# Performance work log

Measured on AMD Instinct MI355X. Metric: run time of the kernel, lower is better.

The kernel has to match this reference:

```python
import jax, jax.numpy as jnp
import numpy as np
from jax import lax

B, H, W, C = 8, 128, 128, 256
HEADS, DH, KR = 8, 64, 64
INNER = HEADS * DH  # 512


def setup_inputs() -> dict:
    key = jax.random.key(0)
    ks = jax.random.split(key, 8)
    s = 0.02
    return {
        "x": jax.random.normal(ks[0], (B, H * W, C), jnp.float32),
        "conv_w": jax.random.normal(ks[1], (INNER, C, 3, 3), jnp.float32) * s,
        "conv_b": jnp.zeros((INNER,), jnp.float32),
        "Wq": jax.random.normal(ks[2], (KR, DH), jnp.float32) * s,
        "Wk": jax.random.normal(ks[3], (KR, DH), jnp.float32) * s,
        "Wv": jax.random.normal(ks[4], (DH, DH), jnp.float32) * s,
        "W1": jax.random.normal(ks[5], (C, INNER), jnp.float32) * s,
        "b1": jnp.zeros((C,), jnp.float32),
        "W2": jax.random.normal(ks[6], (C, C), jnp.float32) * s,
        "b2": jnp.zeros((C,), jnp.float32),
    }


def reference(x, conv_w, conv_b, Wq, Wk, Wv, W1, b1, W2, b2):
    Bv, N, Cv = x.shape
    # b (h w) c -> b c h w
    x4 = x.reshape(Bv, H, W, Cv).transpose(0, 3, 1, 2)
    xc = lax.conv_general_dilated(
        x4, conv_w, window_strides=(1, 1), padding="SAME",
        dimension_numbers=("NCHW", "OIHW", "NCHW"))
    xc = xc + conv_b[None, :, None, None]
    # b (nh dh) h w -> b nh (h w) dh
    x_mid = xc.reshape(Bv, HEADS, DH, H * W).transpose(0, 1, 3, 2)
    q = jnp.einsum("bhnd,kd->bhnk", x_mid, Wq)
    k = jnp.einsum("bhnd,kd->bhnk", x_mid, Wk)
    v = jnp.einsum("bhnd,cd->bhnc", x_mid, Wv)
    q = jax.nn.softmax(q, axis=-1)           # over key_ratio dim
    k = jax.nn.softmax(k, axis=-2)           # over sequence dim
    kv = jnp.einsum("bhnd,bhnc->bhdc", k, v)  # [B,H,KR,DH]
    qkv = jnp.einsum("bhnd,bhdc->bhnc", q, kv)
    # b h n d -> b n (h d)
    qkv = qkv.transpose(0, 2, 1, 3).reshape(Bv, N, INNER)
    h = jax.nn.gelu(qkv @ W1.T + b1, approximate=False)
    return h @ W2.T + b2
```

## Files before the change

### kernel.cpp

```cpp
#include <hip/hip_runtime.h>
#include <math.h>

#define BB 8
#define NN 16384
#define CCH 256
#define OCH 512
#define IMG 128

typedef float4 f4;
typedef _Float16 half8 __attribute__((ext_vector_type(8)));
typedef float floatx4 __attribute__((ext_vector_type(4)));

__device__ __forceinline__ f4 ldg4(const float* p) { return *(const f4*)p; }

__device__ __forceinline__ void gl16(const _Float16* g, const _Float16* l) {
  __builtin_amdgcn_global_load_lds(
      (const __attribute__((address_space(1))) void*)g,
      (__attribute__((address_space(3))) void*)l, 16, 0, 0);
}

__global__ __launch_bounds__(256) void pad_split(const float* __restrict__ x,
                                                 _Float16* __restrict__ xh,
                                                 _Float16* __restrict__ xl) {
  int tid = blockIdx.x * 256 + threadIdx.x;
  int c8 = tid & 31;
  int p = tid >> 5;
  int xcol = p % 130;
  int p2 = p / 130;
  int y = p2 % 130;
  int b = p2 / 130;
  half8 hv, lv;
#pragma unroll
  for (int j = 0; j < 8; ++j) { hv[j] = (_Float16)0.f; lv[j] = (_Float16)0.f; }
  if (y >= 1 && y <= 128 && xcol >= 1 && xcol <= 128) {
    const float* src = x + ((size_t)(b * 128 + y - 1) * 128 + (xcol - 1)) * 256 + c8 * 8;
    f4 v0 = ldg4(src);
    f4 v1 = ldg4(src + 4);
    float vv[8] = {v0.x, v0.y, v0.z, v0.w, v1.x, v1.y, v1.z, v1.w};
#pragma unroll
    for (int j = 0; j < 8; ++j) {
      _Float16 h = (_Float16)vv[j];
      hv[j] = h;
      lv[j] = (_Float16)(vv[j] - (float)h);
    }
  }
  size_t dst = (size_t)p * 256 + c8 * 8;
  *(half8*)(xh + dst) = hv;
  *(half8*)(xl + dst) = lv;
}

__global__ __launch_bounds__(256) void wsplit(const float* __restrict__ cw,
                                              _Float16* __restrict__ wh,
                                              _Float16* __restrict__ wl) {
  int tid = blockIdx.x * 256 + threadIdx.x;
  int c8 = tid & 31;
  int o = (tid >> 5) & 511;
  int tap = tid >> 14;
  half8 hv, lv;
#pragma unroll
  for (int j = 0; j < 8; ++j) {
    float v = cw[(size_t)o * 2304 + (c8 * 8 + j) * 9 + tap];
    _Float16 h = (_Float16)v;
    hv[j] = h;
    lv[j] = (_Float16)(v - (float)h);
  }
  size_t dst = ((size_t)tap * 512 + o) * 256 + c8 * 8;
  *(half8*)(wh + dst) = hv;
  *(half8*)(wl + dst) = lv;
}

__global__ __launch_bounds__(256) void conv_mfma(const _Float16* __restrict__ xph,
                                                 const _Float16* __restrict__ xpl,
                                                 const _Float16* __restrict__ wh,
                                                 const _Float16* __restrict__ wl,
                                                 const float* __restrict__ cb,
                                                 float* __restrict__ xc) {
  __shared__ __align__(16) _Float16 sm[32768];
  const int t = threadIdx.x;
  const int w = t >> 6, lane = t & 63;
  const int id = blockIdx.x;
  const int swz = (id & 7) * 512 + (id >> 3);
  const int obase = (swz & 3) * 128;
  const int p = swz >> 2;
  const int bi = p >> 7, yy = p & 127;
  const int wm = (w & 1) * 64, wn = (w >> 1) * 64;

  floatx4 acc[4][4];
#pragma unroll
  for (int i = 0; i < 4; ++i)
#pragma unroll
    for (int j = 0; j < 4; ++j) acc[i][j] = (floatx4){0.f, 0.f, 0.f, 0.f};

  const int g0 = w, g1 = 4 + w;
  const int loff0 = ((g0 & 1) * 64 + lane) * 256 + (g0 >> 1) * 8;
  const int loff1 = ((g1 & 1) * 64 + lane) * 256 + (g1 >> 1) * 8;

  auto stage = [&](int it, int bsel) {
    const int tap = it >> 3;
    const int dy = (tap * 11) >> 5;
    const int dx = tap - dy * 3;
    const int c0 = (it & 7) * 32;
    const size_t ab = (size_t)((bi * 130 + yy + dy) * 130 + dx) * 256 + c0;
    const size_t bb = (size_t)(tap * 512 + obase) * 256 + c0;
    _Float16* smb = sm + bsel * 16384;
    gl16(xph + ab + loff0, smb + g0 * 512);
    gl16(xph + ab + loff1, smb + g1 * 512);
    gl16(xpl + ab + loff0, smb + 4096 + g0 * 512);
    gl16(xpl + ab + loff1, smb + 4096 + g1 * 512);
    gl16(wh + bb + loff0, smb + 8192 + g0 * 512);
    gl16(wh + bb + loff1, smb + 8192 + g1 * 512);
    gl16(wl + bb + loff0, smb + 12288 + g0 * 512);
    gl16(wl + bb + loff1, smb + 12288 + g1 * 512);
  };

  const int kq = (lane >> 4) * 1024;
  const int ar = (wm + (lane & 15)) * 8;
  const int br = (wn + (lane & 15)) * 8;

  stage(0, 0);
  asm volatile("s_waitcnt vmcnt(0)" ::: "memory");
  __builtin_amdgcn_s_barrier();

  int buf = 0;
#pragma unroll 2
  for (int it = 0; it < 72; ++it) {
    if (it < 71) stage(it + 1, buf ^ 1);

    const _Float16* smb = sm + buf * 16384;
    half8 ah[4], al[4], bh[4], bl[4];
#pragma unroll
    for (int mt = 0; mt < 4; ++mt) {
      ah[mt] = *(const half8*)&smb[kq + ar + mt * 128];
      al[mt] = *(const half8*)&smb[4096 + kq + ar + mt * 128];
    }
#pragma unroll
    for (int nt = 0; nt < 4; ++nt) {
      bh[nt] = *(const half8*)&smb[8192 + kq + br + nt * 128];
      bl[nt] = *(const half8*)&smb[12288 + kq + br + nt * 128];
    }

    __builtin_amdgcn_s_setprio(1);
#pragma unroll
    for (int mt = 0; mt < 4; ++mt)
#pragma unroll
      for (int nt = 0; nt < 4; ++nt) {
        acc[mt][nt] = __builtin_amdgcn_mfma_f32_16x16x32_f16(ah[mt], bh[nt], acc[mt][nt], 0, 0, 0);
        acc[mt][nt] = __builtin_amdgcn_mfma_f32_16x16x32_f16(al[mt], bh[nt], acc[mt][nt], 0, 0, 0);
        acc[mt][nt] = __builtin_amdgcn_mfma_f32_16x16x32_f16(ah[mt], bl[nt], acc[mt][nt], 0, 0, 0);
      }
    __builtin_amdgcn_s_setprio(0);
    __builtin_amdgcn_sched_barrier(0);
    asm volatile("s_waitcnt vmcnt(0)" ::: "memory");
    __builtin_amdgcn_s_barrier();
    buf ^= 1;
  }

  const int col = lane & 15;
  const int qr = (lane >> 4) * 4;
#pragma unroll
  for (int nt = 0; nt < 4; ++nt) {
    const int och = obase + wn + nt * 16 + col;
    const float bias = cb[och];
#pragma unroll
    for (int mt = 0; mt < 4; ++mt)
#pragma unroll
      for (int r = 0; r < 4; ++r) {
        int m = wm + mt * 16 + qr + r;
        xc[((size_t)bi * NN + (size_t)yy * IMG + m) * OCH + och] = acc[mt][nt][r] + bias;
      }
  }
}

__global__ __launch_bounds__(256) void bkern(const float* __restrict__ xc,
                                             const float* __restrict__ Wk,
                                             const float* __restrict__ Wv,
                                             float* __restrict__ P,
                                             float* __restrict__ PS) {
  __shared__ float wkT[4096];
  __shared__ float wvT[4096];
  __shared__ float red[64 * 65];
  __shared__ float Sred[64];
  const int t = threadIdx.x;
  const int bh = blockIdx.x >> 3;
  const int sp = blockIdx.x & 7;
  const int b = bh >> 3, h = bh & 7;
  {
    int d4 = (t & 15) * 4;
#pragma unroll
    for (int p = 0; p < 4; ++p) {
      int kr = (t >> 4) + p * 16;
      f4 wk = ldg4(Wk + kr * 64 + d4);
      f4 wv = ldg4(Wv + kr * 64 + d4);
      wkT[(d4 + 0) * 64 + kr] = wk.x; wkT[(d4 + 1) * 64 + kr] = wk.y;
      wkT[(d4 + 2) * 64 + kr] = wk.z; wkT[(d4 + 3) * 64 + kr] = wk.w;
      wvT[(d4 + 0) * 64 + kr] = wv.x; wvT[(d4 + 1) * 64 + kr] = wv.y;
      wvT[(d4 + 2) * 64 + kr] = wv.z; wvT[(d4 + 3) * 64 + kr] = wv.w;
    }
  }
  __syncthreads();
  const int lane = t & 63, w = t >> 6;
  float macc[64];
#pragma unroll
  for (int d = 0; d < 64; ++d) macc[d] = 0.f;
  float ssum = 0.f;
  const int nbase = sp * 2048 + w * 512;
  const float* xrow = xc + (size_t)(b * NN + nbase) * OCH + h * 64 + lane;
  for (int r = 0; r < 512; ++r) {
    float xv = *xrow;
    xrow += OCH;
    int xi = __float_as_int(xv);
    float klog = 0.f, vv = 0.f;
#pragma unroll
    for (int d = 0; d < 64; ++d) {
      float xd = __int_as_float(__builtin_amdgcn_readlane(xi, d));
      klog = fmaf(xd, wkT[d * 64 + lane], klog);
      vv = fmaf(xd, wvT[d * 64 + lane], vv);
    }
    float ek = expf(klog);
    ssum += ek;
    int ei = __float_as_int(ek);
#pragma unroll
    for (int d = 0; d < 64; ++d) {
      float ekd = __int_as_float(__builtin_amdgcn_readlane(ei, d));
      macc[d] = fmaf(ekd, vv, macc[d]);
    }
  }
  for (int ww = 0; ww < 4; ++ww) {
    if (w == ww) {
      if (ww == 0) {
#pragma unroll
        for (int d = 0; d < 64; ++d) red[d * 65 + lane] = macc[d];
        Sred[lane] = ssum;
      } else {
#pragma unroll
        for (int d = 0; d < 64; ++d) red[d * 65 + lane] += macc[d];
        Sred[lane] += ssum;
      }
    }
    __syncthreads();
  }
  float* Pp = P + (size_t)blockIdx.x * 4096;
#pragma unroll
  for (int e = 0; e < 16; ++e) {
    int idx = t + e * 256;
    Pp[idx] = red[(idx >> 6) * 65 + (idx & 63)];
  }
  if (t < 64) PS[blockIdx.x * 64 + t] = Sred[t];
}

__global__ __launch_bounds__(256) void ckern(const float* __restrict__ P,
                                             const float* __restrict__ PS,
                                             float* __restrict__ kvb) {
  int bh = blockIdx.x, t = threadIdx.x;
#pragma unroll
  for (int e = 0; e < 16; ++e) {
    int idx = t + e * 256;
    int d = idx >> 6;
    float m = 0.f, s = 0.f;
    for (int sp = 0; sp < 8; ++sp) {
      m += P[(size_t)(bh * 8 + sp) * 4096 + idx];
      s += PS[(bh * 8 + sp) * 64 + d];
    }
    kvb[(size_t)bh * 4096 + idx] = m / s;
  }
}

__global__ __launch_bounds__(256) void d1kern(float* __restrict__ xc,
                                              const float* __restrict__ Wq,
                                              const float* __restrict__ kvb) {
  __shared__ float WqT[64 * 68];
  __shared__ float kvs[64 * 68];
  __shared__ float Xs[64 * 68];
  __shared__ float Et[64 * 68];
  __shared__ float rs[64];
  const int t = threadIdx.x;
  const int tx = t & 15, ty = t >> 4;
  const int row0 = blockIdx.x * 64;
  const int b = row0 >> 14;
  {
    int d4 = (t & 15) * 4;
#pragma unroll
    for (int p = 0; p < 4; ++p) {
      int kr = (t >> 4) + p * 16;
      f4 wq = ldg4(Wq + kr * 64 + d4);
      WqT[(d4 + 0) * 68 + kr] = wq.x; WqT[(d4 + 1) * 68 + kr] = wq.y;
      WqT[(d4 + 2) * 68 + kr] = wq.z; WqT[(d4 + 3) * 68 + kr] = wq.w;
    }
  }
  for (int h = 0; h < 8; ++h) {
    __syncthreads();
#pragma unroll
    for (int p = 0; p < 4; ++p) {
      int lin4 = t + p * 256;
      int d = lin4 >> 4;
      int c = (lin4 & 15) * 4;
      f4 kv = ldg4(kvb + (size_t)(b * 8 + h) * 4096 + lin4 * 4);
      *(f4*)&kvs[d * 68 + c] = kv;
    }
    {
      int d4 = (t & 15) * 4;
#pragma unroll
      for (int p = 0; p < 4; ++p) {
        int r = (t >> 4) + p * 16;
        f4 xv = ldg4(xc + (size_t)(row0 + r) * OCH + h * 64 + d4);
        Xs[(d4 + 0) * 68 + r] = xv.x; Xs[(d4 + 1) * 68 + r] = xv.y;
        Xs[(d4 + 2) * 68 + r] = xv.z; Xs[(d4 + 3) * 68 + r] = xv.w;
      }
    }
    __syncthreads();
    float a1[4][4];
#pragma unroll
    for (int i = 0; i < 4; ++i)
#pragma unroll
      for (int j = 0; j < 4; ++j) a1[i][j] = 0.f;
    const f4* Xs4 = (const f4*)Xs;
    const f4* Wq4 = (const f4*)WqT;
#pragma unroll 8
    for (int k = 0; k < 64; ++k) {
      f4 a = Xs4[k * 17 + ty];
      f4 bq = Wq4[k * 17 + tx];
      float av[4] = {a.x, a.y, a.z, a.w};
      float bv[4] = {bq.x, bq.y, bq.z, bq.w};
#pragma unroll
      for (int i = 0; i < 4; ++i)
#pragma unroll
        for (int j = 0; j < 4; ++j) a1[i][j] = fmaf(av[i], bv[j], a1[i][j]);
    }
#pragma unroll
    for (int i = 0; i < 4; ++i)
#pragma unroll
      for (int j = 0; j < 4; ++j)
        Et[(tx * 4 + j) * 68 + ty * 4 + i] = expf(a1[i][j]);
    __syncthreads();
    if (t < 64) {
      float s = 0.f;
      for (int kr = 0; kr < 64; ++kr) s += Et[kr * 68 + t];
      rs[t] = s;
    }
    __syncthreads();
    float a2[4][4];
#pragma unroll
    for (int i = 0; i < 4; ++i)
#pragma unroll
      for (int j = 0; j < 4; ++j) a2[i][j] = 0.f;
    const f4* Et4 = (const f4*)Et;
    const f4* kv4 = (const f4*)kvs;
#pragma unroll 8
    for (int k = 0; k < 64; ++k) {
      f4 a = Et4[k * 17 + ty];
      f4 bv = kv4[k * 17 + tx];
      float av[4] = {a.x, a.y, a.z, a.w};
      float bb[4] = {bv.x, bv.y, bv.z, bv.w};
#pragma unroll
      for (int i = 0; i < 4; ++i)
#pragma unroll
        for (int j = 0; j < 4; ++j) a2[i][j] = fmaf(av[i], bb[j], a2[i][j]);
    }
#pragma unroll
    for (int i = 0; i < 4; ++i) {
      float inv = 1.0f / rs[ty * 4 + i];
      *(f4*)&xc[(size_t)(row0 + ty * 4 + i) * OCH + h * 64 + tx * 4] =
          make_float4(a2[i][0] * inv, a2[i][1] * inv, a2[i][2] * inv, a2[i][3] * inv);
    }
  }
}

template <int KTOT, bool DOGELU>
__global__ __launch_bounds__(256) void mlp(const float* __restrict__ X,
                                           const float* __restrict__ W,
                                           const float* __restrict__ bias,
                                           float* __restrict__ Y) {
  __shared__ float Xs[64 * 132];
  __shared__ float Ws[64 * 132];
  const int t = threadIdx.x;
  const int tx = t & 15, ty = t >> 4;
  const int jbase = blockIdx.x * 128;
  const int row0 = blockIdx.y * 128;
  float acc[8][8];
#pragma unroll
  for (int i = 0; i < 8; ++i)
#pragma unroll
    for (int j = 0; j < 8; ++j) acc[i][j] = 0.f;
  const int d4 = (t & 15) * 4;
  for (int kc = 0; kc < KTOT / 64; ++kc) {
    int kb = kc * 64;
    __syncthreads();
#pragma unroll
    for (int p = 0; p < 8; ++p) {
      int r = (t >> 4) + p * 16;
      f4 xv = ldg4(X + (size_t)(row0 + r) * KTOT + kb + d4);
      Xs[(d4 + 0) * 132 + r] = xv.x; Xs[(d4 + 1) * 132 + r] = xv.y;
      Xs[(d4 + 2) * 132 + r] = xv.z; Xs[(d4 + 3) * 132 + r] = xv.w;
    }
#pragma unroll
    for (int p = 0; p < 8; ++p) {
      int jj = (t >> 4) + p * 16;
      f4 wv = ldg4(W + (size_t)(jbase + jj) * KTOT + kb + d4);
      Ws[(d4 + 0) * 132 + jj] = wv.x; Ws[(d4 + 1) * 132 + jj] = wv.y;
      Ws[(d4 + 2) * 132 + jj] = wv.z; Ws[(d4 + 3) * 132 + jj] = wv.w;
    }
    __syncthreads();
    const f4* Xs4 = (const f4*)Xs;
    const f4* Ws4 = (const f4*)Ws;
#pragma unroll 8
    for (int k = 0; k < 64; ++k) {
      f4 a0 = Xs4[k * 33 + ty * 2];
      f4 a1 = Xs4[k * 33 + ty * 2 + 1];
      f4 b0 = Ws4[k * 33 + tx * 2];
      f4 b1 = Ws4[k * 33 + tx * 2 + 1];
      float a[8] = {a0.x, a0.y, a0.z, a0.w, a1.x, a1.y, a1.z, a1.w};
      float b[8] = {b0.x, b0.y, b0.z, b0.w, b1.x, b1.y, b1.z, b1.w};
#pragma unroll
      for (int i = 0; i < 8; ++i)
#pragma unroll
        for (int j = 0; j < 8; ++j) acc[i][j] = fmaf(a[i], b[j], acc[i][j]);
    }
  }
  float bb[8];
#pragma unroll
  for (int j = 0; j < 8; ++j) bb[j] = bias[jbase + tx * 8 + j];
#pragma unroll
  for (int i = 0; i < 8; ++i) {
    int row = row0 + ty * 8 + i;
    float v[8];
#pragma unroll
    for (int j = 0; j < 8; ++j) {
      v[j] = acc[i][j] + bb[j];
      if (DOGELU) v[j] = 0.5f * v[j] * (1.0f + erff(v[j] * 0.70710678118654752440f));
    }
    *(f4*)&Y[(size_t)row * 256 + jbase + tx * 8] = make_float4(v[0], v[1], v[2], v[3]);
    *(f4*)&Y[(size_t)row * 256 + jbase + tx * 8 + 4] = make_float4(v[4], v[5], v[6], v[7]);
  }
}

extern "C" void kernel_launch(void* const* d_in, const int* in_sizes, int n_in,
                              void* d_out, int out_size, void* d_ws, size_t ws_size,
                              hipStream_t stream) {
  const float* x  = (const float*)d_in[0];
  const float* cw = (const float*)d_in[1];
  const float* cb = (const float*)d_in[2];
  const float* Wq = (const float*)d_in[3];
  const float* Wk = (const float*)d_in[4];
  const float* Wv = (const float*)d_in[5];
  const float* W1 = (const float*)d_in[6];
  const float* b1 = (const float*)d_in[7];
  const float* W2 = (const float*)d_in[8];
  const float* b2 = (const float*)d_in[9];
  float* out = (float*)d_out;
  float* ws = (float*)d_ws;

  _Float16* xph = (_Float16*)ws;
  _Float16* xpl = (_Float16*)(ws + 17305600);
  float* P   = ws;
  float* PS  = ws + 2097152;
  float* kvb = ws + 2129920;
  float* y1w = ws;
  float* xc  = ws + 34611200;
  _Float16* wh = (_Float16*)(ws + 101720064);
  _Float16* wl = (_Float16*)(ws + 102309888);

  pad_split<<<16900, 256, 0, stream>>>(x, xph, xpl);
  wsplit<<<576, 256, 0, stream>>>(cw, wh, wl);
  conv_mfma<<<4096, 256, 0, stream>>>(xph, xpl, wh, wl, cb, xc);
  bkern<<<512, 256, 0, stream>>>(xc, Wk, Wv, P, PS);
  ckern<<<64, 256, 0, stream>>>(P, PS, kvb);
  d1kern<<<2048, 256, 0, stream>>>(xc, Wq, kvb);
  mlp<512, true><<<dim3(2, 1024), 256, 0, stream>>>(xc, W1, b1, y1w);
  mlp<256, false><<<dim3(2, 1024), 256, 0, stream>>>(y1w, W2, b2, out);
}
```

Baseline: 3.269 ms.

## Triple-buffer conv MFMA K-loop with partial vmcnt waits

Grows the conv kernel's shared-memory staging from two to three buffers so each iteration prefetches two steps ahead. Global-to-LDS loads are issued after the LDS fragment reads, and each step waits only on the older batch (vmcnt(8)) instead of draining all loads. The MFMA sequence is also regrouped into three passes over the 16 tiles to expose independent accumulator chains. This raises LDS use from 64KB to 96KB per block, which may reduce occupancy.

After: 3.345 ms. 1.02x slower.

```diff
diff --git a/kernel.cpp b/kernel.cpp
--- a/kernel.cpp
+++ b/kernel.cpp
@@ -75,7 +75,7 @@
                                                  const _Float16* __restrict__ wl,
                                                  const float* __restrict__ cb,
                                                  float* __restrict__ xc) {
-  __shared__ __align__(16) _Float16 sm[32768];
+  __shared__ __align__(16) _Float16 sm[49152];
   const int t = threadIdx.x;
   const int w = t >> 6, lane = t & 63;
   const int id = blockIdx.x;
@@ -95,14 +95,13 @@
   const int loff0 = ((g0 & 1) * 64 + lane) * 256 + (g0 >> 1) * 8;
   const int loff1 = ((g1 & 1) * 64 + lane) * 256 + (g1 >> 1) * 8;
 
-  auto stage = [&](int it, int bsel) {
+  auto stage = [&](int it, _Float16* smb) {
     const int tap = it >> 3;
     const int dy = (tap * 11) >> 5;
     const int dx = tap - dy * 3;
     const int c0 = (it & 7) * 32;
     const size_t ab = (size_t)((bi * 130 + yy + dy) * 130 + dx) * 256 + c0;
     const size_t bb = (size_t)(tap * 512 + obase) * 256 + c0;
-    _Float16* smb = sm + bsel * 16384;
     gl16(xph + ab + loff0, smb + g0 * 512);
     gl16(xph + ab + loff1, smb + g1 * 512);
     gl16(xpl + ab + loff0, smb + 4096 + g0 * 512);
@@ -117,16 +116,7 @@
   const int ar = (wm + (lane & 15)) * 8;
   const int br = (wn + (lane & 15)) * 8;
 
-  stage(0, 0);
-  asm volatile("s_waitcnt vmcnt(0)" ::: "memory");
-  __builtin_amdgcn_s_barrier();
-
-  int buf = 0;
-#pragma unroll 2
-  for (int it = 0; it < 72; ++it) {
-    if (it < 71) stage(it + 1, buf ^ 1);
-
-    const _Float16* smb = sm + buf * 16384;
+  auto kstep = [&](const _Float16* smb, int sit, _Float16* sdst, bool dostg) {
     half8 ah[4], al[4], bh[4], bl[4];
 #pragma unroll
     for (int mt = 0; mt < 4; ++mt) {
@@ -138,22 +128,46 @@
       bh[nt] = *(const half8*)&smb[8192 + kq + br + nt * 128];
       bl[nt] = *(const half8*)&smb[12288 + kq + br + nt * 128];
     }
-
+    if (dostg) stage(sit, sdst);
+    __builtin_amdgcn_sched_barrier(0);
     __builtin_amdgcn_s_setprio(1);
 #pragma unroll
     for (int mt = 0; mt < 4; ++mt)
 #pragma unroll
-      for (int nt = 0; nt < 4; ++nt) {
+      for (int nt = 0; nt < 4; ++nt)
         acc[mt][nt] = __builtin_amdgcn_mfma_f32_16x16x32_f16(ah[mt], bh[nt], acc[mt][nt], 0, 0, 0);
+#pragma unroll
+    for (int mt = 0; mt < 4; ++mt)
+#pragma unroll
+      for (int nt = 0; nt < 4; ++nt)
         acc[mt][nt] = __builtin_amdgcn_mfma_f32_16x16x32_f16(al[mt], bh[nt], acc[mt][nt], 0, 0, 0);
+#pragma unroll
+    for (int mt = 0; mt < 4; ++mt)
+#pragma unroll
+      for (int nt = 0; nt < 4; ++nt)
         acc[mt][nt] = __builtin_amdgcn_mfma_f32_16x16x32_f16(ah[mt], bl[nt], acc[mt][nt], 0, 0, 0);
-      }
     __builtin_amdgcn_s_setprio(0);
-    __builtin_amdgcn_sched_barrier(0);
-    asm volatile("s_waitcnt vmcnt(0)" ::: "memory");
-    __builtin_amdgcn_s_barrier();
-    buf ^= 1;
-  }
+  };
+
+#define HEADW(N)                                              \
+  do {                                                        \
+    asm volatile("s_waitcnt vmcnt(" #N ")" ::: "memory");     \
+    __builtin_amdgcn_s_barrier();                             \
+  } while (0)
+
+  stage(0, sm);
+  stage(1, sm + 16384);
+
+  for (int m = 0; m < 23; ++m) {
+    const int it = m * 3;
+    HEADW(8); kstep(sm,         it + 2, sm + 32768, true);
+    HEADW(8); kstep(sm + 16384, it + 3, sm,         true);
+    HEADW(8); kstep(sm + 32768, it + 4, sm + 16384, true);
+  }
+  HEADW(8); kstep(sm,         71, sm + 32768, true);
+  HEADW(8); kstep(sm + 16384, 0, (_Float16*)0, false);
+  HEADW(0); kstep(sm + 32768, 0, (_Float16*)0, false);
+#undef HEADW
 
   const int col = lane & 15;
   const int qr = (lane >> 4) * 4;
```

## Use 512-thread blocks in conv MFMA with smaller per-wave tiles

Applied to the files above, without the earlier changes.

The conv implicit-GEMM kernel now runs 8 waves per block instead of 4. Each wave computes a 32x64 output sub-tile instead of 64x64, which halves the accumulator registers and the A-fragment loads per wave, and each wave issues one global-to-LDS load per matrix instead of two. The three MFMA passes (hi*hi, lo*hi, hi*lo) are regrouped so that consecutive MFMAs write independent accumulators. The aim is to raise occupancy and latency hiding. The cost is that B fragments are now loaded redundantly by more waves and barrier synchronisation covers twice as many waves.

Result: slower. 3.483 ms (+6.6%).

```diff
diff --git a/kernel.cpp b/kernel.cpp
--- a/kernel.cpp
+++ b/kernel.cpp
@@ -69,12 +69,12 @@
   *(half8*)(wl + dst) = lv;
 }
 
-__global__ __launch_bounds__(256) void conv_mfma(const _Float16* __restrict__ xph,
-                                                 const _Float16* __restrict__ xpl,
-                                                 const _Float16* __restrict__ wh,
-                                                 const _Float16* __restrict__ wl,
-                                                 const float* __restrict__ cb,
-                                                 float* __restrict__ xc) {
+__global__ __launch_bounds__(512, 4) void conv_mfma(const _Float16* __restrict__ xph,
+                                                    const _Float16* __restrict__ xpl,
+                                                    const _Float16* __restrict__ wh,
+                                                    const _Float16* __restrict__ wl,
+                                                    const float* __restrict__ cb,
+                                                    float* __restrict__ xc) {
   __shared__ __align__(16) _Float16 sm[32768];
   const int t = threadIdx.x;
   const int w = t >> 6, lane = t & 63;
@@ -83,53 +83,46 @@
   const int obase = (swz & 3) * 128;
   const int p = swz >> 2;
   const int bi = p >> 7, yy = p & 127;
-  const int wm = (w & 1) * 64, wn = (w >> 1) * 64;
-
-  floatx4 acc[4][4];
-#pragma unroll
-  for (int i = 0; i < 4; ++i)
+  const int wm = (w & 3) * 32, wn = (w >> 2) * 64;
+
+  floatx4 acc[2][4];
+#pragma unroll
+  for (int i = 0; i < 2; ++i)
 #pragma unroll
     for (int j = 0; j < 4; ++j) acc[i][j] = (floatx4){0.f, 0.f, 0.f, 0.f};
 
-  const int g0 = w, g1 = 4 + w;
-  const int loff0 = ((g0 & 1) * 64 + lane) * 256 + (g0 >> 1) * 8;
-  const int loff1 = ((g1 & 1) * 64 + lane) * 256 + (g1 >> 1) * 8;
-
-  auto stage = [&](int it, int bsel) {
+  const int loff = ((w & 1) * 64 + lane) * 256 + (w >> 1) * 8;
+  const int ldst = w * 512;
+
+  auto stage = [&](int it, _Float16* smb) {
     const int tap = it >> 3;
     const int dy = (tap * 11) >> 5;
     const int dx = tap - dy * 3;
     const int c0 = (it & 7) * 32;
-    const size_t ab = (size_t)((bi * 130 + yy + dy) * 130 + dx) * 256 + c0;
-    const size_t bb = (size_t)(tap * 512 + obase) * 256 + c0;
-    _Float16* smb = sm + bsel * 16384;
-    gl16(xph + ab + loff0, smb + g0 * 512);
-    gl16(xph + ab + loff1, smb + g1 * 512);
-    gl16(xpl + ab + loff0, smb + 4096 + g0 * 512);
-    gl16(xpl + ab + loff1, smb + 4096 + g1 * 512);
-    gl16(wh + bb + loff0, smb + 8192 + g0 * 512);
-    gl16(wh + bb + loff1, smb + 8192 + g1 * 512);
-    gl16(wl + bb + loff0, smb + 12288 + g0 * 512);
-    gl16(wl + bb + loff1, smb + 12288 + g1 * 512);
+    const size_t ab = (size_t)((bi * 130 + yy + dy) * 130 + dx) * 256 + c0 + loff;
+    const size_t bb = (size_t)(tap * 512 + obase) * 256 + c0 + loff;
+    gl16(xph + ab, smb + ldst);
+    gl16(xpl + ab, smb + 4096 + ldst);
+    gl16(wh + bb, smb + 8192 + ldst);
+    gl16(wl + bb, smb + 12288 + ldst);
   };
 
   const int kq = (lane >> 4) * 1024;
   const int ar = (wm + (lane & 15)) * 8;
   const int br = (wn + (lane & 15)) * 8;
 
-  stage(0, 0);
+  stage(0, sm);
   asm volatile("s_waitcnt vmcnt(0)" ::: "memory");
   __builtin_amdgcn_s_barrier();
 
-  int buf = 0;
 #pragma unroll 2
   for (int it = 0; it < 72; ++it) {
-    if (it < 71) stage(it + 1, buf ^ 1);
-
-    const _Float16* smb = sm + buf * 16384;
-    half8 ah[4], al[4], bh[4], bl[4];
-#pragma unroll
-    for (int mt = 0; mt < 4; ++mt) {
+    _Float16* smb = sm + (it & 1) * 16384;
+    if (it < 71) stage(it + 1, sm + ((it + 1) & 1) * 16384);
+
+    half8 ah[2], al[2], bh[4], bl[4];
+#pragma unroll
+    for (int mt = 0; mt < 2; ++mt) {
       ah[mt] = *(const half8*)&smb[kq + ar + mt * 128];
       al[mt] = *(const half8*)&smb[4096 + kq + ar + mt * 128];
     }
@@ -141,18 +134,24 @@
 
     __builtin_amdgcn_s_setprio(1);
 #pragma unroll
-    for (int mt = 0; mt < 4; ++mt)
-#pragma unroll
-      for (int nt = 0; nt < 4; ++nt) {
+    for (int mt = 0; mt < 2; ++mt)
+#pragma unroll
+      for (int nt = 0; nt < 4; ++nt)
         acc[mt][nt] = __builtin_amdgcn_mfma_f32_16x16x32_f16(ah[mt], bh[nt], acc[mt][nt], 0, 0, 0);
+#pragma unroll
+    for (int mt = 0; mt < 2; ++mt)
+#pragma unroll
+      for (int nt = 0; nt < 4; ++nt)
         acc[mt][nt] = __builtin_amdgcn_mfma_f32_16x16x32_f16(al[mt], bh[nt], acc[mt][nt], 0, 0, 0);
+#pragma unroll
+    for (int mt = 0; mt < 2; ++mt)
+#pragma unroll
+      for (int nt = 0; nt < 4; ++nt)
         acc[mt][nt] = __builtin_amdgcn_mfma_f32_16x16x32_f16(ah[mt], bl[nt], acc[mt][nt], 0, 0, 0);
-      }
     __builtin_amdgcn_s_setprio(0);
     __builtin_amdgcn_sched_barrier(0);
     asm volatile("s_waitcnt vmcnt(0)" ::: "memory");
     __builtin_amdgcn_s_barrier();
-    buf ^= 1;
   }
 
   const int col = lane & 15;
@@ -162,7 +161,7 @@
     const int och = obase + wn + nt * 16 + col;
     const float bias = cb[och];
 #pragma unroll
-    for (int mt = 0; mt < 4; ++mt)
+    for (int mt = 0; mt < 2; ++mt)
 #pragma unroll
       for (int r = 0; r < 4; ++r) {
         int m = wm + mt * 16 + qr + r;
@@ -461,7 +460,7 @@
 
   pad_split<<<16900, 256, 0, stream>>>(x, xph, xpl);
   wsplit<<<576, 256, 0, stream>>>(cw, wh, wl);
-  conv_mfma<<<4096, 256, 0, stream>>>(xph, xpl, wh, wl, cb, xc);
+  conv_mfma<<<4096, 512, 0, stream>>>(xph, xpl, wh, wl, cb, xc);
   bkern<<<512, 256, 0, stream>>>(xc, Wk, Wv, P, PS);
   ckern<<<64, 256, 0, stream>>>(P, PS, kvb);
   d1kern<<<2048, 256, 0, stream>>>(xc, Wq, kvb);
```

## Move MLP GEMMs to split-fp16 MFMA with packed hi/lo activations

Applied to the files above, without the earlier changes.

Replaces the two fp32 SIMT MLP GEMMs with MFMA kernels that use the same three-term fp16 hi/lo split as the conv. The attention output and the GELU output are written as packed hi/lo fp16 pairs, so the MLP kernels read them directly. The W1 and W2 weights are split into hi/lo arrays by a new small kernel. A tile is double-buffered, with the A operand staged through registers and the B operand loaded straight into LDS. The split scheme carries some accuracy risk, and two extra launches are added.

After: 2.702 ms. -17.3%, faster.

```diff
diff --git a/kernel.cpp b/kernel.cpp
--- a/kernel.cpp
+++ b/kernel.cpp
@@ -17,6 +17,28 @@
   __builtin_amdgcn_global_load_lds(
       (const __attribute__((address_space(1))) void*)g,
       (__attribute__((address_space(3))) void*)l, 16, 0, 0);
+}
+
+__device__ __forceinline__ uint32_t packhl(float v) {
+  _Float16 h = (_Float16)v;
+  _Float16 l = (_Float16)(v - (float)h);
+  unsigned short hu, lu;
+  __builtin_memcpy(&hu, &h, 2);
+  __builtin_memcpy(&lu, &l, 2);
+  return (uint32_t)hu | ((uint32_t)lu << 16);
+}
+__device__ __forceinline__ _Float16 lo16h(uint32_t u) {
+  unsigned short s = (unsigned short)(u & 0xffffu);
+  _Float16 h; __builtin_memcpy(&h, &s, 2); return h;
+}
+__device__ __forceinline__ _Float16 hi16h(uint32_t u) {
+  unsigned short s = (unsigned short)(u >> 16);
+  _Float16 h; __builtin_memcpy(&h, &s, 2); return h;
+}
+__device__ __forceinline__ void unpack8(uint4 a, uint4 b, half8& hv, half8& lv) {
+  uint32_t wv[8] = {a.x, a.y, a.z, a.w, b.x, b.y, b.z, b.w};
+#pragma unroll
+  for (int j = 0; j < 8; ++j) { hv[j] = lo16h(wv[j]); lv[j] = hi16h(wv[j]); }
 }
 
 __global__ __launch_bounds__(256) void pad_split(const float* __restrict__ x,
@@ -67,6 +89,27 @@
   size_t dst = ((size_t)tap * 512 + o) * 256 + c8 * 8;
   *(half8*)(wh + dst) = hv;
   *(half8*)(wl + dst) = lv;
+}
+
+__global__ __launch_bounds__(256) void wsplit_lin(const float* __restrict__ W,
+                                                  _Float16* __restrict__ wh,
+                                                  _Float16* __restrict__ wl,
+                                                  int n8) {
+  int tid = blockIdx.x * 256 + threadIdx.x;
+  if (tid >= n8) return;
+  const float* src = W + (size_t)tid * 8;
+  f4 v0 = ldg4(src);
+  f4 v1 = ldg4(src + 4);
+  float vv[8] = {v0.x, v0.y, v0.z, v0.w, v1.x, v1.y, v1.z, v1.w};
+  half8 hv, lv;
+#pragma unroll
+  for (int j = 0; j < 8; ++j) {
+    _Float16 h = (_Float16)vv[j];
+    hv[j] = h;
+    lv[j] = (_Float16)(vv[j] - (float)h);
+  }
+  *(half8*)(wh + (size_t)tid * 8) = hv;
+  *(half8*)(wl + (size_t)tid * 8) = lv;
 }
 
 __global__ __launch_bounds__(256) void conv_mfma(const _Float16* __restrict__ xph,
@@ -95,14 +138,13 @@
   const int loff0 = ((g0 & 1) * 64 + lane) * 256 + (g0 >> 1) * 8;
   const int loff1 = ((g1 & 1) * 64 + lane) * 256 + (g1 >> 1) * 8;
 
-  auto stage = [&](int it, int bsel) {
+  auto stage = [&](int it, _Float16* smb) {
     const int tap = it >> 3;
     const int dy = (tap * 11) >> 5;
     const int dx = tap - dy * 3;
     const int c0 = (it & 7) * 32;
     const size_t ab = (size_t)((bi * 130 + yy + dy) * 130 + dx) * 256 + c0;
     const size_t bb = (size_t)(tap * 512 + obase) * 256 + c0;
-    _Float16* smb = sm + bsel * 16384;
     gl16(xph + ab + loff0, smb + g0 * 512);
     gl16(xph + ab + loff1, smb + g1 * 512);
     gl16(xpl + ab + loff0, smb + 4096 + g0 * 512);
@@ -117,16 +159,15 @@
   const int ar = (wm + (lane & 15)) * 8;
   const int br = (wn + (lane & 15)) * 8;
 
-  stage(0, 0);
+  stage(0, sm);
   asm volatile("s_waitcnt vmcnt(0)" ::: "memory");
   __builtin_amdgcn_s_barrier();
 
-  int buf = 0;
 #pragma unroll 2
   for (int it = 0; it < 72; ++it) {
-    if (it < 71) stage(it + 1, buf ^ 1);
-
-    const _Float16* smb = sm + buf * 16384;
+    _Float16* smb = sm + (it & 1) * 16384;
+    if (it < 71) stage(it + 1, sm + ((it + 1) & 1) * 16384);
+
     half8 ah[4], al[4], bh[4], bl[4];
 #pragma unroll
     for (int mt = 0; mt < 4; ++mt) {
@@ -152,7 +193,6 @@
     __builtin_amdgcn_sched_barrier(0);
     asm volatile("s_waitcnt vmcnt(0)" ::: "memory");
     __builtin_amdgcn_s_barrier();
-    buf ^= 1;
   }
 
   const int col = lane & 15;
@@ -359,77 +399,142 @@
 #pragma unroll
     for (int i = 0; i < 4; ++i) {
       float inv = 1.0f / rs[ty * 4 + i];
-      *(f4*)&xc[(size_t)(row0 + ty * 4 + i) * OCH + h * 64 + tx * 4] =
-          make_float4(a2[i][0] * inv, a2[i][1] * inv, a2[i][2] * inv, a2[i][3] * inv);
+      uint32_t pw0 = packhl(a2[i][0] * inv);
+      uint32_t pw1 = packhl(a2[i][1] * inv);
+      uint32_t pw2 = packhl(a2[i][2] * inv);
+      uint32_t pw3 = packhl(a2[i][3] * inv);
+      *(uint4*)&((uint32_t*)xc)[(size_t)(row0 + ty * 4 + i) * OCH + h * 64 + tx * 4] =
+          make_uint4(pw0, pw1, pw2, pw3);
     }
   }
 }
 
 template <int KTOT, bool DOGELU>
-__global__ __launch_bounds__(256) void mlp(const float* __restrict__ X,
-                                           const float* __restrict__ W,
-                                           const float* __restrict__ bias,
-                                           float* __restrict__ Y) {
-  __shared__ float Xs[64 * 132];
-  __shared__ float Ws[64 * 132];
+__global__ __launch_bounds__(256) void mlp_mfma(const uint32_t* __restrict__ Xp,
+                                                const _Float16* __restrict__ bwh,
+                                                const _Float16* __restrict__ bwl,
+                                                const float* __restrict__ bias,
+                                                void* __restrict__ Yout) {
+  __shared__ __align__(16) _Float16 sm[32768];
   const int t = threadIdx.x;
-  const int tx = t & 15, ty = t >> 4;
+  const int w = t >> 6, lane = t & 63;
   const int jbase = blockIdx.x * 128;
   const int row0 = blockIdx.y * 128;
-  float acc[8][8];
-#pragma unroll
-  for (int i = 0; i < 8; ++i)
-#pragma unroll
-    for (int j = 0; j < 8; ++j) acc[i][j] = 0.f;
-  const int d4 = (t & 15) * 4;
-  for (int kc = 0; kc < KTOT / 64; ++kc) {
-    int kb = kc * 64;
-    __syncthreads();
-#pragma unroll
-    for (int p = 0; p < 8; ++p) {
-      int r = (t >> 4) + p * 16;
-      f4 xv = ldg4(X + (size_t)(row0 + r) * KTOT + kb + d4);
-      Xs[(d4 + 0) * 132 + r] = xv.x; Xs[(d4 + 1) * 132 + r] = xv.y;
-      Xs[(d4 + 2) * 132 + r] = xv.z; Xs[(d4 + 3) * 132 + r] = xv.w;
-    }
-#pragma unroll
-    for (int p = 0; p < 8; ++p) {
-      int jj = (t >> 4) + p * 16;
-      f4 wv = ldg4(W + (size_t)(jbase + jj) * KTOT + kb + d4);
-      Ws[(d4 + 0) * 132 + jj] = wv.x; Ws[(d4 + 1) * 132 + jj] = wv.y;
-      Ws[(d4 + 2) * 132 + jj] = wv.z; Ws[(d4 + 3) * 132 + jj] = wv.w;
-    }
-    __syncthreads();
-    const f4* Xs4 = (const f4*)Xs;
-    const f4* Ws4 = (const f4*)Ws;
-#pragma unroll 8
-    for (int k = 0; k < 64; ++k) {
-      f4 a0 = Xs4[k * 33 + ty * 2];
-      f4 a1 = Xs4[k * 33 + ty * 2 + 1];
-      f4 b0 = Ws4[k * 33 + tx * 2];
-      f4 b1 = Ws4[k * 33 + tx * 2 + 1];
-      float a[8] = {a0.x, a0.y, a0.z, a0.w, a1.x, a1.y, a1.z, a1.w};
-      float b[8] = {b0.x, b0.y, b0.z, b0.w, b1.x, b1.y, b1.z, b1.w};
-#pragma unroll
-      for (int i = 0; i < 8; ++i)
-#pragma unroll
-        for (int j = 0; j < 8; ++j) acc[i][j] = fmaf(a[i], b[j], acc[i][j]);
-    }
-  }
-  float bb[8];
-#pragma unroll
-  for (int j = 0; j < 8; ++j) bb[j] = bias[jbase + tx * 8 + j];
-#pragma unroll
-  for (int i = 0; i < 8; ++i) {
-    int row = row0 + ty * 8 + i;
-    float v[8];
-#pragma unroll
-    for (int j = 0; j < 8; ++j) {
-      v[j] = acc[i][j] + bb[j];
-      if (DOGELU) v[j] = 0.5f * v[j] * (1.0f + erff(v[j] * 0.70710678118654752440f));
-    }
-    *(f4*)&Y[(size_t)row * 256 + jbase + tx * 8] = make_float4(v[0], v[1], v[2], v[3]);
-    *(f4*)&Y[(size_t)row * 256 + jbase + tx * 8 + 4] = make_float4(v[4], v[5], v[6], v[7]);
+  const int wm = (w & 1) * 64, wn = (w >> 1) * 64;
+  constexpr int KS = KTOT / 32;
+
+  floatx4 acc[4][4];
+#pragma unroll
+  for (int i = 0; i < 4; ++i)
+#pragma unroll
+    for (int j = 0; j < 4; ++j) acc[i][j] = (floatx4){0.f, 0.f, 0.f, 0.f};
+
+  const int g0 = w, g1 = 4 + w;
+  const int loff0 = ((g0 & 1) * 64 + lane) * KTOT + (g0 >> 1) * 8;
+  const int loff1 = ((g1 & 1) * 64 + lane) * KTOT + (g1 >> 1) * 8;
+  const int rowA = t & 127, kk0 = t >> 7, kk1 = (t >> 7) + 2;
+  const uint32_t* arow = Xp + (size_t)(row0 + rowA) * KTOT;
+
+  const int kq = (lane >> 4) * 1024;
+  const int ar = (wm + (lane & 15)) * 8;
+  const int br = (wn + (lane & 15)) * 8;
+
+  {
+    uint4 a0l = *(const uint4*)(arow + kk0 * 8);
+    uint4 a0h = *(const uint4*)(arow + kk0 * 8 + 4);
+    uint4 a1l = *(const uint4*)(arow + kk1 * 8);
+    uint4 a1h = *(const uint4*)(arow + kk1 * 8 + 4);
+    const size_t bb = (size_t)jbase * KTOT;
+    gl16(bwh + bb + loff0, sm + 8192 + g0 * 512);
+    gl16(bwh + bb + loff1, sm + 8192 + g1 * 512);
+    gl16(bwl + bb + loff0, sm + 12288 + g0 * 512);
+    gl16(bwl + bb + loff1, sm + 12288 + g1 * 512);
+    half8 hv, lv;
+    unpack8(a0l, a0h, hv, lv);
+    *(half8*)&sm[kk0 * 1024 + rowA * 8] = hv;
+    *(half8*)&sm[4096 + kk0 * 1024 + rowA * 8] = lv;
+    unpack8(a1l, a1h, hv, lv);
+    *(half8*)&sm[kk1 * 1024 + rowA * 8] = hv;
+    *(half8*)&sm[4096 + kk1 * 1024 + rowA * 8] = lv;
+  }
+  asm volatile("s_waitcnt vmcnt(0) lgkmcnt(0)" ::: "memory");
+  __builtin_amdgcn_s_barrier();
+
+#pragma unroll 2
+  for (int kt = 0; kt < KS; ++kt) {
+    _Float16* smb = sm + (kt & 1) * 16384;
+    _Float16* nbuf = sm + ((kt + 1) & 1) * 16384;
+    const bool pre = (kt < KS - 1);
+    uint4 a0l, a0h, a1l, a1h;
+    if (pre) {
+      const int kbn = (kt + 1) * 32;
+      a0l = *(const uint4*)(arow + kbn + kk0 * 8);
+      a0h = *(const uint4*)(arow + kbn + kk0 * 8 + 4);
+      a1l = *(const uint4*)(arow + kbn + kk1 * 8);
+      a1h = *(const uint4*)(arow + kbn + kk1 * 8 + 4);
+      const size_t bb = (size_t)jbase * KTOT + kbn;
+      gl16(bwh + bb + loff0, nbuf + 8192 + g0 * 512);
+      gl16(bwh + bb + loff1, nbuf + 8192 + g1 * 512);
+      gl16(bwl + bb + loff0, nbuf + 12288 + g0 * 512);
+      gl16(bwl + bb + loff1, nbuf + 12288 + g1 * 512);
+    }
+
+    half8 ah[4], al[4], bh[4], bl[4];
+#pragma unroll
+    for (int mt = 0; mt < 4; ++mt) {
+      ah[mt] = *(const half8*)&smb[kq + ar + mt * 128];
+      al[mt] = *(const half8*)&smb[4096 + kq + ar + mt * 128];
+    }
+#pragma unroll
+    for (int nt = 0; nt < 4; ++nt) {
+      bh[nt] = *(const half8*)&smb[8192 + kq + br + nt * 128];
+      bl[nt] = *(const half8*)&smb[12288 + kq + br + nt * 128];
+    }
+
+    __builtin_amdgcn_s_setprio(1);
+#pragma unroll
+    for (int mt = 0; mt < 4; ++mt)
+#pragma unroll
+      for (int nt = 0; nt < 4; ++nt) {
+        acc[mt][nt] = __builtin_amdgcn_mfma_f32_16x16x32_f16(ah[mt], bh[nt], acc[mt][nt], 0, 0, 0);
+        acc[mt][nt] = __builtin_amdgcn_mfma_f32_16x16x32_f16(al[mt], bh[nt], acc[mt][nt], 0, 0, 0);
+        acc[mt][nt] = __builtin_amdgcn_mfma_f32_16x16x32_f16(ah[mt], bl[nt], acc[mt][nt], 0, 0, 0);
+      }
+    __builtin_amdgcn_s_setprio(0);
+
+    if (pre) {
+      half8 hv, lv;
+      unpack8(a0l, a0h, hv, lv);
+      *(half8*)&nbuf[kk0 * 1024 + rowA * 8] = hv;
+      *(half8*)&nbuf[4096 + kk0 * 1024 + rowA * 8] = lv;
+      unpack8(a1l, a1h, hv, lv);
+      *(half8*)&nbuf[kk1 * 1024 + rowA * 8] = hv;
+      *(half8*)&nbuf[4096 + kk1 * 1024 + rowA * 8] = lv;
+    }
+    __builtin_amdgcn_sched_barrier(0);
+    asm volatile("s_waitcnt vmcnt(0) lgkmcnt(0)" ::: "memory");
+    __builtin_amdgcn_s_barrier();
+  }
+
+  const int col = lane & 15;
+  const int qr = (lane >> 4) * 4;
+#pragma unroll
+  for (int nt = 0; nt < 4; ++nt) {
+    const int j = jbase + wn + nt * 16 + col;
+    const float bj = bias[j];
+#pragma unroll
+    for (int mt = 0; mt < 4; ++mt)
+#pragma unroll
+      for (int r = 0; r < 4; ++r) {
+        const int row = row0 + wm + mt * 16 + qr + r;
+        float v = acc[mt][nt][r] + bj;
+        if (DOGELU) {
+          v = 0.5f * v * (1.0f + erff(v * 0.70710678118654752440f));
+          ((uint32_t*)Yout)[(size_t)row * 256 + j] = packhl(v);
+        } else {
+          ((float*)Yout)[(size_t)row * 256 + j] = v;
+        }
+      }
   }
 }
 
@@ -454,7 +559,12 @@
   float* P   = ws;
   float* PS  = ws + 2097152;
   float* kvb = ws + 2129920;
-  float* y1w = ws;
+  uint32_t* y1p = (uint32_t*)ws;
+  _Float16* mw = (_Float16*)(ws + 33554432);
+  _Float16* wh1 = mw;
+  _Float16* wl1 = mw + 131072;
+  _Float16* wh2 = mw + 262144;
+  _Float16* wl2 = mw + 327680;
   float* xc  = ws + 34611200;
   _Float16* wh = (_Float16*)(ws + 101720064);
   _Float16* wl = (_Float16*)(ws + 102309888);
@@ -462,9 +572,11 @@
   pad_split<<<16900, 256, 0, stream>>>(x, xph, xpl);
   wsplit<<<576, 256, 0, stream>>>(cw, wh, wl);
   conv_mfma<<<4096, 256, 0, stream>>>(xph, xpl, wh, wl, cb, xc);
+  wsplit_lin<<<64, 256, 0, stream>>>(W1, wh1, wl1, 16384);
+  wsplit_lin<<<32, 256, 0, stream>>>(W2, wh2, wl2, 8192);
   bkern<<<512, 256, 0, stream>>>(xc, Wk, Wv, P, PS);
   ckern<<<64, 256, 0, stream>>>(P, PS, kvb);
   d1kern<<<2048, 256, 0, stream>>>(xc, Wq, kvb);
-  mlp<512, true><<<dim3(2, 1024), 256, 0, stream>>>(xc, W1, b1, y1w);
-  mlp<256, false><<<dim3(2, 1024), 256, 0, stream>>>(y1w, W2, b2, out);
-}
+  mlp_mfma<512, true><<<dim3(2, 1024), 256, 0, stream>>>((const uint32_t*)xc, wh1, wl1, b1, y1p);
+  mlp_mfma<256, false><<<dim3(2, 1024), 256, 0, stream>>>(y1p, wh2, wl2, b2, out);
+}
```
